# Performance work log

Hardware: AMD Instinct MI355X
Metric: run time of the kernel (lower is better)

Reference implementation:

```python
import jax, jax.numpy as jnp
import numpy as np

EPS = 1e-5  # torch InstanceNorm2d default eps


def setup_inputs() -> dict:
    key = jax.random.key(0)
    ks = jax.random.split(key, 5)
    B, C, H, W = 4, 64, 64, 64
    x = jax.random.normal(ks[0], (B, C, H, W), dtype=jnp.float32)
    # Conv2d 1x1 weights as [out_c, in_c] matrices (kernel dims squeezed)
    w_qkv = jax.random.normal(ks[1], (3 * C, C), dtype=jnp.float32) * (C ** -0.5)
    b_qkv = jax.random.normal(ks[2], (3 * C,), dtype=jnp.float32) * 0.02
    w_proj = jax.random.normal(ks[3], (C, C), dtype=jnp.float32) * (C ** -0.5)
    b_proj = jax.random.normal(ks[4], (C,), dtype=jnp.float32) * 0.02
    return {"x": x, "w_qkv": w_qkv, "b_qkv": b_qkv, "w_proj": w_proj, "b_proj": b_proj}


def reference(x, w_qkv, b_qkv, w_proj, b_proj):
    B, C, H, W = x.shape
    scale = C ** -0.5
    # InstanceNorm2d(affine=False): per-(B,C) stats over spatial dims, biased var
    mean = jnp.mean(x, axis=(2, 3), keepdims=True)
    var = jnp.var(x, axis=(2, 3), keepdims=True)
    h = (x - mean) * jax.lax.rsqrt(var + EPS)
    # 1x1 conv qkv projection: [B,3C,H,W]
    qkv = jnp.einsum('bchw,oc->bohw', h, w_qkv) + b_qkv[None, :, None, None]
    q, k, v = jnp.split(qkv, 3, axis=1)
    HW = H * W
    q = q.reshape(B, C, HW).transpose(0, 2, 1)  # [B, HW, C]
    k = k.reshape(B, C, HW)                      # [B, C, HW]
    v = v.reshape(B, C, HW).transpose(0, 2, 1)  # [B, HW, C]
    attn = jnp.einsum('bnc,bcm->bnm', q, k) * scale  # [B, HW, HW]
    attn = jax.nn.softmax(attn, axis=-1)
    # dropout p=0.0 -> identity
    h = jnp.einsum('bnm,bmc->bnc', attn, v)          # [B, HW, C]
    h = h.transpose(0, 2, 1).reshape(B, C, H, W)
    h = jnp.einsum('bchw,oc->bohw', h, w_proj) + b_proj[None, :, None, None]
    return x + h
```

## Files before the change

kernel.cpp:

```cpp
#include <hip/hip_runtime.h>
#include <hip/hip_bf16.h>

#define B_ 4
#define C_ 64
#define N_ 4096
#define EPS_ 1e-5f
#define C2_ 0.18033688011112042f

typedef __hip_bfloat16 bf16;
typedef __attribute__((ext_vector_type(8))) short short8;
typedef __attribute__((ext_vector_type(4))) short short4v;
typedef __attribute__((ext_vector_type(4))) float f32x4;

__device__ __forceinline__ float b2f(bf16 v) { return __bfloat162float(v); }

__device__ __forceinline__ short f2bs(float f) {
  union { bf16 h; short s; } u;
  u.h = __float2bfloat16(f);
  return u.s;
}

__device__ __forceinline__ short8 pk8(const float* f) {
  union { short8 v; short s[8]; } u;
#pragma unroll
  for (int i = 0; i < 8; ++i) u.s[i] = f2bs(f[i]);
  return u.v;
}

__device__ __forceinline__ void up8(short8 v, float* d) {
  union { short8 v; unsigned u[4]; } x;
  x.v = v;
  d[0] = __uint_as_float(x.u[0] << 16);
  d[1] = __uint_as_float(x.u[0] & 0xffff0000u);
  d[2] = __uint_as_float(x.u[1] << 16);
  d[3] = __uint_as_float(x.u[1] & 0xffff0000u);
  d[4] = __uint_as_float(x.u[2] << 16);
  d[5] = __uint_as_float(x.u[2] & 0xffff0000u);
  d[6] = __uint_as_float(x.u[3] << 16);
  d[7] = __uint_as_float(x.u[3] & 0xffff0000u);
}

__device__ __forceinline__ void up4(ushort4 u, float* d) {
  d[0] = __uint_as_float(((unsigned)u.x) << 16);
  d[1] = __uint_as_float(((unsigned)u.y) << 16);
  d[2] = __uint_as_float(((unsigned)u.z) << 16);
  d[3] = __uint_as_float(((unsigned)u.w) << 16);
}

template <bool F32>
__device__ __forceinline__ float ldx(const void* p, size_t idx) {
  if (F32) return ((const float*)p)[idx];
  return b2f(((const bf16*)p)[idx]);
}

template <bool F32>
__device__ __forceinline__ short8 ld8(const void* p, int idx) {
  if (F32) {
    const float* fp = (const float*)p + idx;
    float tmp[8];
    *(float4*)&tmp[0] = *(const float4*)fp;
    *(float4*)&tmp[4] = *(const float4*)(fp + 4);
    return pk8(tmp);
  }
  return *(const short8*)((const bf16*)p + idx);
}

__device__ __forceinline__ f32x4 mfma32(short8 a, short8 b, f32x4 c) {
  return __builtin_amdgcn_mfma_f32_16x16x32_bf16(a, b, c, 0, 0, 0);
}
__device__ __forceinline__ f32x4 mfma16(short4v a, short4v b, f32x4 c) {
  return __builtin_amdgcn_mfma_f32_16x16x16bf16_1k(a, b, c, 0, 0, 0);
}


template <bool F32>
__device__ __forceinline__ void stats_sum(const void* x, int bc, int t,
                                          float& s, float& s2) {
  if (F32) {
    const float4* xp = (const float4*)((const float*)x + (size_t)bc * N_);
#pragma unroll
    for (int r = 0; r < 4; ++r) {
      const float4 v = xp[r * 256 + t];
      s += (v.x + v.y) + (v.z + v.w);
      s2 += (v.x * v.x + v.y * v.y) + (v.z * v.z + v.w * v.w);
    }
  } else {
    const bf16* xp = (const bf16*)x + (size_t)bc * N_;
#pragma unroll
    for (int r = 0; r < 2; ++r) {
      float f[8];
      up8(*(const short8*)(xp + (r * 256 + t) * 8), f);
#pragma unroll
      for (int i = 0; i < 8; ++i) { s += f[i]; s2 += f[i] * f[i]; }
    }
  }
}

__global__ __launch_bounds__(256) void k_stats(const void* __restrict__ x,
                                               float* __restrict__ meanArr,
                                               float* __restrict__ rstdArr,
                                               int* __restrict__ flag) {
  const int bc = blockIdx.x, t = threadIdx.x;
  __shared__ float ps[4], ps2[4];
  __shared__ int pflag;
  {
    const ushort* xw = (const ushort*)x + (size_t)bc * 4096;
    int cnt = 0;
#pragma unroll
    for (int j = 0; j < 4; ++j) {
      const ushort4 u = *(const ushort4*)(xw + t * 16 + j * 4);
      cnt += ((u.x >> 7) & 0xFF) >= 143;
      cnt += ((u.y >> 7) & 0xFF) >= 143;
      cnt += ((u.z >> 7) & 0xFF) >= 143;
      cnt += ((u.w >> 7) & 0xFF) >= 143;
    }
#pragma unroll
    for (int off = 32; off > 0; off >>= 1) cnt += __shfl_down(cnt, off, 64);
    if (t == 0) pflag = 0;
    __syncthreads();
    if ((t & 63) == 0 && cnt > 16) atomicAdd(&pflag, cnt);
    __syncthreads();
  }
  const bool f32 = pflag > 64;
  float s = 0.f, s2 = 0.f;
  if (f32) stats_sum<true>(x, bc, t, s, s2);
  else stats_sum<false>(x, bc, t, s, s2);
#pragma unroll
  for (int off = 32; off > 0; off >>= 1) {
    s += __shfl_down(s, off, 64);
    s2 += __shfl_down(s2, off, 64);
  }
  if ((t & 63) == 0) { ps[t >> 6] = s; ps2[t >> 6] = s2; }
  __syncthreads();
  if (t == 0) {
    const float S = (ps[0] + ps[1]) + (ps[2] + ps[3]);
    const float S2 = (ps2[0] + ps2[1]) + (ps2[2] + ps2[3]);
    const float mean = S * (1.0f / N_);
    const float var = S2 * (1.0f / N_) - mean * mean;
    meanArr[bc] = mean;
    rstdArr[bc] = rsqrtf(var + EPS_);
    flag[0] = f32 ? 1 : 0;
  }
}

template <bool F32>
__device__ __forceinline__ void qkv_body(const void* x, const void* wqkv,
                                         const void* bqkv, const float* meanArr,
                                         const float* rstdArr, bf16* q, bf16* k,
                                         bf16* v, short* HB) {
  const int t = threadIdx.x, tj = blockIdx.x, b = blockIdx.y;
  const int n0 = tj * 64;
  {
    const int li = t & 15, nbt = (t >> 4) & 3, cg = t >> 6;
    const int n = n0 + nbt * 16 + li;
    const float* mb_ = meanArr + b * 64;
    const float* rb_ = rstdArr + b * 64;
    float hv[16];
#pragma unroll
    for (int i = 0; i < 16; ++i) {
      const int c = cg * 16 + i;
      hv[i] = (ldx<F32>(x, ((size_t)(b * 64 + c)) * N_ + n) - mb_[c]) * rb_[c];
    }
#pragma unroll
    for (int c8 = 0; c8 < 2; ++c8) {
      const int ks = cg >> 1, qd = (cg & 1) * 2 + c8;
      *(short8*)&HB[((nbt * 2 + ks) * 64 + qd * 16 + li) * 8] = pk8(&hv[c8 * 8]);
    }
  }
  __syncthreads();
  const int l = t & 63, w = t >> 6, li = l & 15, quad = l >> 4;
  short8 Wf[3][2];
#pragma unroll
  for (int sec = 0; sec < 3; ++sec)
#pragma unroll
    for (int ks = 0; ks < 2; ++ks)
      Wf[sec][ks] = ld8<F32>(wqkv, (sec * 64 + w * 16 + li) * 64 + ks * 32 + quad * 8);
  short8 Hf[4][2];
#pragma unroll
  for (int nb = 0; nb < 4; ++nb)
#pragma unroll
    for (int ks = 0; ks < 2; ++ks)
      Hf[nb][ks] = *(const short8*)&HB[((nb * 2 + ks) * 64 + l) * 8];
  float bq[4], bk[4];
#pragma unroll
  for (int r = 0; r < 4; ++r) {
    bq[r] = ldx<F32>(bqkv, w * 16 + quad * 4 + r);
    bk[r] = ldx<F32>(bqkv, 64 + w * 16 + quad * 4 + r);
  }
  const float bv = ldx<F32>(bqkv, 128 + w * 16 + li);
  const int lhi = ((w & 1) * 2 + (quad >> 1)) * 16 + li;
  const int jj0 = (quad & 1) * 4;
#pragma unroll
  for (int nb = 0; nb < 4; ++nb) {
    f32x4 dq = {0.f, 0.f, 0.f, 0.f}, dk = dq, dv = dq;
    dq = mfma32(Wf[0][0], Hf[nb][0], dq);
    dq = mfma32(Wf[0][1], Hf[nb][1], dq);
    dk = mfma32(Wf[1][0], Hf[nb][0], dk);
    dk = mfma32(Wf[1][1], Hf[nb][1], dk);
    dv = mfma32(Hf[nb][0], Wf[2][0], dv);
    dv = mfma32(Hf[nb][1], Wf[2][1], dv);
    union { ushort4 u; short s[4]; } pq, pk_, pv;
#pragma unroll
    for (int r = 0; r < 4; ++r) {
      pq.s[r] = f2bs(dq[r] + bq[r]);
      pk_.s[r] = f2bs(dk[r] + bk[r]);
      pv.s[r] = f2bs(dv[r] + bv);
    }
    *(ushort4*)&q[(((size_t)(b * 256 + tj * 4 + nb)) * 2 + (w >> 1)) * 512 + lhi * 8 + jj0] = pq.u;
    *(ushort4*)&k[(((size_t)(b * 64 + tj)) * 8 + nb * 2 + (w >> 1)) * 512 + lhi * 8 + jj0] = pk_.u;
    *(ushort4*)&v[(((size_t)(b * 64 + tj)) * 16 + w * 4 + nb) * 256 + (quad * 16 + li) * 4] = pv.u;
  }
}
__global__ __launch_bounds__(256) void k_qkv(
    const void* __restrict__ x, const void* __restrict__ wqkv,
    const void* __restrict__ bqkv, const float* __restrict__ meanArr,
    const float* __restrict__ rstdArr, bf16* __restrict__ q,
    bf16* __restrict__ k, bf16* __restrict__ v, const int* __restrict__ flag) {
  __shared__ short HB[4096];
  if (*flag) qkv_body<true>(x, wqkv, bqkv, meanArr, rstdArr, q, k, v, HB);
  else qkv_body<false>(x, wqkv, bqkv, meanArr, rstdArr, q, k, v, HB);
}

__device__ __forceinline__ void stage(short* dst, const bf16* ks_,
                                      const bf16* vs_, int w, int ln) {
#pragma unroll
  for (int i = 0; i < 2; ++i) {
    const int off = w * 1024 + i * 512;
    __builtin_amdgcn_global_load_lds(
        (const __attribute__((address_space(1))) unsigned int*)(ks_ + off + ln * 8),
        (__attribute__((address_space(3))) unsigned int*)(dst + off), 16, 0, 0);
    __builtin_amdgcn_global_load_lds(
        (const __attribute__((address_space(1))) unsigned int*)(vs_ + off + ln * 8),
        (__attribute__((address_space(3))) unsigned int*)(dst + 4096 + off), 16, 0, 0);
  }
}

__global__ __launch_bounds__(256, 2) void k_attn(
    const bf16* __restrict__ qg, const bf16* __restrict__ kg,
    const bf16* __restrict__ vg, bf16* __restrict__ opart,
    float* __restrict__ lpart) {
  __shared__ __align__(16) short KV[2][8192];
  const int bid = blockIdx.x;
  const int g = bid & 7, s = bid >> 3;
  const int c = g * 2 + (s & 1);
  const int b = c & 3, kh = c >> 2, qt = s >> 1;
  const int t = threadIdx.x, l = t & 63, w = t >> 6, li = l & 15, quad = l >> 4;

  short8 Qf[2][2];
#pragma unroll
  for (int q = 0; q < 2; ++q)
#pragma unroll
    for (int ks = 0; ks < 2; ++ks)
      Qf[q][ks] = *(const short8*)(qg +
          (((size_t)(b * 256 + qt * 8 + w * 2 + q)) * 2 + ks) * 512 + l * 8);

  f32x4 O[4][2];
#pragma unroll
  for (int cb = 0; cb < 4; ++cb)
#pragma unroll
    for (int q = 0; q < 2; ++q) O[cb][q] = {0.f, 0.f, 0.f, 0.f};
  float ls[2] = {0.f, 0.f};

  const bf16* kbase = kg + ((size_t)(b * 64 + kh * 16)) * 4096;
  const bf16* vbase = vg + ((size_t)(b * 64 + kh * 16)) * 4096;

  stage(&KV[0][0], kbase, vbase, w, l);
  __syncthreads();
  for (int it = 0; it < 16; ++it) {
    const short* buf = &KV[it & 1][0];
    if (it + 1 < 16)
      stage(&KV[(it + 1) & 1][0], kbase + (size_t)(it + 1) * 4096,
            vbase + (size_t)(it + 1) * 4096, w, l);
    short8 Kf[4][2];
#pragma unroll
    for (int jb = 0; jb < 4; ++jb)
#pragma unroll
      for (int ks = 0; ks < 2; ++ks)
        Kf[jb][ks] = *(const short8*)&buf[(jb * 2 + ks) * 512 + l * 8];
    short4v Vf[4][4];
#pragma unroll
    for (int cb = 0; cb < 4; ++cb)
#pragma unroll
      for (int jb = 0; jb < 4; ++jb)
        Vf[cb][jb] = *(const short4v*)&buf[4096 + (cb * 4 + jb) * 256 + l * 4];
#pragma unroll
    for (int jb = 0; jb < 4; ++jb) {
      short4v Pf[2];
#pragma unroll
      for (int q = 0; q < 2; ++q) {
        f32x4 sv = {0.f, 0.f, 0.f, 0.f};
        sv = mfma32(Kf[jb][0], Qf[q][0], sv);
        sv = mfma32(Kf[jb][1], Qf[q][1], sv);
        const float p0 = exp2f(sv[0] * C2_), p1 = exp2f(sv[1] * C2_);
        const float p2 = exp2f(sv[2] * C2_), p3 = exp2f(sv[3] * C2_);
        ls[q] += (p0 + p1) + (p2 + p3);
        union { short4v v; __hip_bfloat162 h[2]; } pu;
        pu.h[0] = __float22bfloat162_rn(make_float2(p0, p1));
        pu.h[1] = __float22bfloat162_rn(make_float2(p2, p3));
        Pf[q] = pu.v;
      }
#pragma unroll
      for (int cb = 0; cb < 4; ++cb)
#pragma unroll
        for (int q = 0; q < 2; ++q)
          O[cb][q] = mfma16(Vf[cb][jb], Pf[q], O[cb][q]);
    }
    __syncthreads();
  }
#pragma unroll
  for (int q = 0; q < 2; ++q) {
    ls[q] += __shfl_xor(ls[q], 16, 64);
    ls[q] += __shfl_xor(ls[q], 32, 64);
  }
  const size_t pb = ((size_t)(kh * 4 + b)) * 32 + qt;
  if (l < 16) {
    lpart[pb * 128 + (w * 2 + 0) * 16 + l] = ls[0];
    lpart[pb * 128 + (w * 2 + 1) * 16 + l] = ls[1];
  }
#pragma unroll
  for (int q = 0; q < 2; ++q)
#pragma unroll
    for (int cb = 0; cb < 4; ++cb) {
      union { ushort4 u; short s[4]; } pk_;
#pragma unroll
      for (int r = 0; r < 4; ++r) pk_.s[r] = f2bs(O[cb][q][r]);
      *(ushort4*)&opart[pb * 8192 + (((w * 2 + q) * 4 + cb) << 8) + l * 4] = pk_.u;
    }
}

template <bool F32>
__device__ __forceinline__ void proj_body(const bf16* opart, const float* lpart,
                                          const void* xg, const void* wp,
                                          const void* bp, void* outv) {
  const int qt64 = blockIdx.x, bb = blockIdx.y;
  const int qt = qt64 >> 1, mbo = (qt64 & 1) * 4;
  const int t = threadIdx.x, l = t & 63, w = t >> 6, li = l & 15, quad = l >> 4;
  short8 Wa[2];
#pragma unroll
  for (int ks = 0; ks < 2; ++ks)
    Wa[ks] = ld8<F32>(wp, (w * 16 + li) * 64 + ks * 32 + quad * 8);
  float bpv[4];
#pragma unroll
  for (int r = 0; r < 4; ++r) bpv[r] = ldx<F32>(bp, w * 16 + quad * 4 + r);
  f32x4 D[4];
#pragma unroll
  for (int mb = 0; mb < 4; ++mb) {
    const int mbg = mbo + mb;
    float lv = 0.f;
#pragma unroll
    for (int p = 0; p < 4; ++p)
      lv += lpart[(((size_t)(p * 4 + bb)) * 32 + qt) * 128 + mbg * 16 + li];
    lv = 1.0f / lv;
    f32x4 acc = {0.f, 0.f, 0.f, 0.f};
#pragma unroll
    for (int ks = 0; ks < 2; ++ks) {
      const int cb = ks * 2 + (quad >> 1);
      const int qs0 = (quad & 1) * 2;
      float s8[8] = {};
#pragma unroll
      for (int p = 0; p < 4; ++p) {
        const size_t base =
            (((size_t)(p * 4 + bb)) * 32 + qt) * 8192 + ((mbg * 4 + cb) << 8);
        float f0[4], f1[4];
        up4(*(const ushort4*)&opart[base + (qs0 * 16 + li) * 4], f0);
        up4(*(const ushort4*)&opart[base + ((qs0 + 1) * 16 + li) * 4], f1);
#pragma unroll
        for (int i = 0; i < 4; ++i) { s8[i] += f0[i]; s8[4 + i] += f1[i]; }
      }
#pragma unroll
      for (int i = 0; i < 8; ++i) s8[i] *= lv;
      acc = mfma32(Wa[ks], pk8(s8), acc);
    }
    D[mb] = acc;
  }
#pragma unroll
  for (int mb = 0; mb < 4; ++mb)
#pragma unroll
    for (int r = 0; r < 4; ++r) {
      const int o = w * 16 + quad * 4 + r;
      const int n = qt64 * 64 + mb * 16 + li;
      const size_t idx = ((size_t)(bb * 64 + o)) * N_ + n;
      const float res = ldx<F32>(xg, idx) + D[mb][r] + bpv[r];
      if (F32) ((float*)outv)[idx] = res;
      else ((bf16*)outv)[idx] = __float2bfloat16(res);
    }
}
__global__ __launch_bounds__(256) void k_proj(
    const bf16* __restrict__ opart, const float* __restrict__ lpart,
    const void* __restrict__ xg, const void* __restrict__ wp,
    const void* __restrict__ bp, void* __restrict__ outv,
    const int* __restrict__ flag) {
  if (*flag) proj_body<true>(opart, lpart, xg, wp, bp, outv);
  else proj_body<false>(opart, lpart, xg, wp, bp, outv);
}

extern "C" void kernel_launch(void* const* d_in, const int* in_sizes, int n_in,
                              void* d_out, int out_size, void* d_ws,
                              size_t ws_size, hipStream_t stream) {
  const void* x = d_in[0];
  const void* wqkv = d_in[1];
  const void* bqkv = d_in[2];
  const void* wproj = d_in[3];
  const void* bproj = d_in[4];

  char* ws = (char*)d_ws;
  float* meanArr = (float*)ws;
  float* rstdArr = (float*)(ws + 1024);
  int* flag = (int*)(ws + 2048);
  bf16* q = (bf16*)(ws + 4096);
  bf16* k = (bf16*)(ws + 4096 + (2u << 20));
  bf16* v = (bf16*)(ws + 4096 + (4u << 20));
  bf16* opart = (bf16*)(ws + 4096 + (6u << 20));
  float* lpart = (float*)(ws + 4096 + (14u << 20));

  k_stats<<<256, 256, 0, stream>>>(x, meanArr, rstdArr, flag);
  k_qkv<<<dim3(64, 4), 256, 0, stream>>>(x, wqkv, bqkv, meanArr, rstdArr, q, k,
                                         v, flag);
  k_attn<<<512, 256, 0, stream>>>(q, k, v, opart, lpart);
  k_proj<<<dim3(64, 4), 256, 0, stream>>>(opart, lpart, x, wproj, bproj, d_out,
                                          flag);
}
```

Measured before the change: 113.3 us.

## Double per-block query tile, split keys 8 ways, prescale Q, pack V loads

Each attention block now handles 64 queries per wave group (4 query fragments per wave) instead of 32, and the key dimension is split into 8 partitions of 512 keys instead of 4 of 1024. This doubles reuse of each K/V tile staged in LDS and halves the iterations per block. The softmax scale is folded into Q at projection time, which removes a multiply per score. V is stored so that 8-element LDS reads replace 4-element ones. The trade-off is more accumulator registers, which may cut occupancy, and twice as many partial outputs for the projection kernel to reduce.

```diff
diff --git a/kernel.cpp b/kernel.cpp
--- a/kernel.cpp
+++ b/kernel.cpp
@@ -202,13 +202,13 @@
     union { ushort4 u; short s[4]; } pq, pk_, pv;
 #pragma unroll
     for (int r = 0; r < 4; ++r) {
-      pq.s[r] = f2bs(dq[r] + bq[r]);
+      pq.s[r] = f2bs((dq[r] + bq[r]) * C2_);
       pk_.s[r] = f2bs(dk[r] + bk[r]);
       pv.s[r] = f2bs(dv[r] + bv);
     }
     *(ushort4*)&q[(((size_t)(b * 256 + tj * 4 + nb)) * 2 + (w >> 1)) * 512 + lhi * 8 + jj0] = pq.u;
     *(ushort4*)&k[(((size_t)(b * 64 + tj)) * 8 + nb * 2 + (w >> 1)) * 512 + lhi * 8 + jj0] = pk_.u;
-    *(ushort4*)&v[(((size_t)(b * 64 + tj)) * 16 + w * 4 + nb) * 256 + (quad * 16 + li) * 4] = pv.u;
+    *(ushort4*)&v[(((size_t)(b * 64 + tj)) * 8 + w * 2 + (nb >> 1)) * 512 + l * 8 + (nb & 1) * 4] = pv.u;
   }
 }
 __global__ __launch_bounds__(256) void k_qkv(
@@ -241,34 +241,33 @@
     float* __restrict__ lpart) {
   __shared__ __align__(16) short KV[2][8192];
   const int bid = blockIdx.x;
-  const int g = bid & 7, s = bid >> 3;
-  const int c = g * 2 + (s & 1);
-  const int b = c & 3, kh = c >> 2, qt = s >> 1;
+  const int kh = bid & 7, s = bid >> 3;
+  const int b = s & 3, qt = s >> 2;
   const int t = threadIdx.x, l = t & 63, w = t >> 6, li = l & 15, quad = l >> 4;
 
-  short8 Qf[2][2];
-#pragma unroll
-  for (int q = 0; q < 2; ++q)
+  short8 Qf[4][2];
+#pragma unroll
+  for (int q = 0; q < 4; ++q)
 #pragma unroll
     for (int ks = 0; ks < 2; ++ks)
       Qf[q][ks] = *(const short8*)(qg +
-          (((size_t)(b * 256 + qt * 8 + w * 2 + q)) * 2 + ks) * 512 + l * 8);
-
-  f32x4 O[4][2];
+          (((size_t)(b * 256 + qt * 16 + w * 4 + q)) * 2 + ks) * 512 + l * 8);
+
+  f32x4 O[4][4];
 #pragma unroll
   for (int cb = 0; cb < 4; ++cb)
 #pragma unroll
-    for (int q = 0; q < 2; ++q) O[cb][q] = {0.f, 0.f, 0.f, 0.f};
-  float ls[2] = {0.f, 0.f};
-
-  const bf16* kbase = kg + ((size_t)(b * 64 + kh * 16)) * 4096;
-  const bf16* vbase = vg + ((size_t)(b * 64 + kh * 16)) * 4096;
+    for (int q = 0; q < 4; ++q) O[cb][q] = {0.f, 0.f, 0.f, 0.f};
+  float ls[4] = {0.f, 0.f, 0.f, 0.f};
+
+  const bf16* kbase = kg + ((size_t)(b * 64 + kh * 8)) * 4096;
+  const bf16* vbase = vg + ((size_t)(b * 64 + kh * 8)) * 4096;
 
   stage(&KV[0][0], kbase, vbase, w, l);
   __syncthreads();
-  for (int it = 0; it < 16; ++it) {
+  for (int it = 0; it < 8; ++it) {
     const short* buf = &KV[it & 1][0];
-    if (it + 1 < 16)
+    if (it + 1 < 8)
       stage(&KV[(it + 1) & 1][0], kbase + (size_t)(it + 1) * 4096,
             vbase + (size_t)(it + 1) * 4096, w, l);
     short8 Kf[4][2];
@@ -277,22 +276,22 @@
 #pragma unroll
       for (int ks = 0; ks < 2; ++ks)
         Kf[jb][ks] = *(const short8*)&buf[(jb * 2 + ks) * 512 + l * 8];
-    short4v Vf[4][4];
+    short8 Vp[4][2];
 #pragma unroll
     for (int cb = 0; cb < 4; ++cb)
 #pragma unroll
-      for (int jb = 0; jb < 4; ++jb)
-        Vf[cb][jb] = *(const short4v*)&buf[4096 + (cb * 4 + jb) * 256 + l * 4];
+      for (int jp = 0; jp < 2; ++jp)
+        Vp[cb][jp] = *(const short8*)&buf[4096 + (cb * 2 + jp) * 512 + l * 8];
 #pragma unroll
     for (int jb = 0; jb < 4; ++jb) {
-      short4v Pf[2];
-#pragma unroll
-      for (int q = 0; q < 2; ++q) {
+      short4v Pf[4];
+#pragma unroll
+      for (int q = 0; q < 4; ++q) {
         f32x4 sv = {0.f, 0.f, 0.f, 0.f};
         sv = mfma32(Kf[jb][0], Qf[q][0], sv);
         sv = mfma32(Kf[jb][1], Qf[q][1], sv);
-        const float p0 = exp2f(sv[0] * C2_), p1 = exp2f(sv[1] * C2_);
-        const float p2 = exp2f(sv[2] * C2_), p3 = exp2f(sv[3] * C2_);
+        const float p0 = exp2f(sv[0]), p1 = exp2f(sv[1]);
+        const float p2 = exp2f(sv[2]), p3 = exp2f(sv[3]);
         ls[q] += (p0 + p1) + (p2 + p3);
         union { short4v v; __hip_bfloat162 h[2]; } pu;
         pu.h[0] = __float22bfloat162_rn(make_float2(p0, p1));
@@ -300,31 +299,36 @@
         Pf[q] = pu.v;
       }
 #pragma unroll
-      for (int cb = 0; cb < 4; ++cb)
-#pragma unroll
-        for (int q = 0; q < 2; ++q)
-          O[cb][q] = mfma16(Vf[cb][jb], Pf[q], O[cb][q]);
+      for (int cb = 0; cb < 4; ++cb) {
+        const short8 vp = Vp[cb][jb >> 1];
+        const short4v vh = (jb & 1)
+            ? __builtin_shufflevector(vp, vp, 4, 5, 6, 7)
+            : __builtin_shufflevector(vp, vp, 0, 1, 2, 3);
+#pragma unroll
+        for (int q = 0; q < 4; ++q) O[cb][q] = mfma16(vh, Pf[q], O[cb][q]);
+      }
     }
     __syncthreads();
   }
 #pragma unroll
-  for (int q = 0; q < 2; ++q) {
+  for (int q = 0; q < 4; ++q) {
     ls[q] += __shfl_xor(ls[q], 16, 64);
     ls[q] += __shfl_xor(ls[q], 32, 64);
   }
-  const size_t pb = ((size_t)(kh * 4 + b)) * 32 + qt;
+  const size_t pb = ((size_t)(kh * 4 + b)) * 16 + qt;
   if (l < 16) {
-    lpart[pb * 128 + (w * 2 + 0) * 16 + l] = ls[0];
-    lpart[pb * 128 + (w * 2 + 1) * 16 + l] = ls[1];
-  }
-#pragma unroll
-  for (int q = 0; q < 2; ++q)
+#pragma unroll
+    for (int q = 0; q < 4; ++q)
+      lpart[(pb * 16 + w * 4 + q) * 16 + l] = ls[q];
+  }
+#pragma unroll
+  for (int q = 0; q < 4; ++q)
 #pragma unroll
     for (int cb = 0; cb < 4; ++cb) {
       union { ushort4 u; short s[4]; } pk_;
 #pragma unroll
       for (int r = 0; r < 4; ++r) pk_.s[r] = f2bs(O[cb][q][r]);
-      *(ushort4*)&opart[pb * 8192 + (((w * 2 + q) * 4 + cb) << 8) + l * 4] = pk_.u;
+      *(ushort4*)&opart[((pb * 16 + w * 4 + q) * 4 + cb) * 256 + l * 4] = pk_.u;
     }
 }
 
@@ -333,7 +337,7 @@
                                           const void* xg, const void* wp,
                                           const void* bp, void* outv) {
   const int qt64 = blockIdx.x, bb = blockIdx.y;
-  const int qt = qt64 >> 1, mbo = (qt64 & 1) * 4;
+  const int qt = qt64 >> 2;
   const int t = threadIdx.x, l = t & 63, w = t >> 6, li = l & 15, quad = l >> 4;
   short8 Wa[2];
 #pragma unroll
@@ -345,11 +349,11 @@
   f32x4 D[4];
 #pragma unroll
   for (int mb = 0; mb < 4; ++mb) {
-    const int mbg = mbo + mb;
+    const int mbg = (qt64 & 3) * 4 + mb;
     float lv = 0.f;
 #pragma unroll
-    for (int p = 0; p < 4; ++p)
-      lv += lpart[(((size_t)(p * 4 + bb)) * 32 + qt) * 128 + mbg * 16 + li];
+    for (int p = 0; p < 8; ++p)
+      lv += lpart[((((size_t)(p * 4 + bb)) * 16 + qt) * 16 + mbg) * 16 + li];
     lv = 1.0f / lv;
     f32x4 acc = {0.f, 0.f, 0.f, 0.f};
 #pragma unroll
@@ -358,9 +362,9 @@
       const int qs0 = (quad & 1) * 2;
       float s8[8] = {};
 #pragma unroll
-      for (int p = 0; p < 4; ++p) {
+      for (int p = 0; p < 8; ++p) {
         const size_t base =
-            (((size_t)(p * 4 + bb)) * 32 + qt) * 8192 + ((mbg * 4 + cb) << 8);
+            (((((size_t)(p * 4 + bb)) * 16 + qt) * 16 + mbg) * 4 + cb) * 256;
         float f0[4], f1[4];
         up4(*(const ushort4*)&opart[base + (qs0 * 16 + li) * 4], f0);
         up4(*(const ushort4*)&opart[base + ((qs0 + 1) * 16 + li) * 4], f1);
@@ -411,7 +415,7 @@
   bf16* k = (bf16*)(ws + 4096 + (2u << 20));
   bf16* v = (bf16*)(ws + 4096 + (4u << 20));
   bf16* opart = (bf16*)(ws + 4096 + (6u << 20));
-  float* lpart = (float*)(ws + 4096 + (14u << 20));
+  float* lpart = (float*)(ws + 4096 + (23u << 20));
 
   k_stats<<<256, 256, 0, stream>>>(x, meanArr, rstdArr, flag);
   k_qkv<<<dim3(64, 4), 256, 0, stream>>>(x, wqkv, bqkv, meanArr, rstdArr, q, k,
```

Measured after the change: 119.5 us. +5.5%, slower.

## Split attention keys into eight chunks, fold softmax scale into Q, repack V

Applied to the files above, without the earlier changes.

The attention kernel now splits the key dimension into 8 partitions instead of 4, launching 1024 blocks with 8 iterations each and a higher occupancy hint. The softmax scale is folded into Q at projection time, which removes a multiply per score. V is stored in a packed 8-wide layout so each wave loads fewer, wider LDS vectors per pair of key blocks, and K fragments are loaded just in time to cut register pressure. The cost is larger partial-output buffers and twice as many partials for the projection kernel to reduce.

```diff
diff --git a/kernel.cpp b/kernel.cpp
--- a/kernel.cpp
+++ b/kernel.cpp
@@ -202,13 +202,13 @@
     union { ushort4 u; short s[4]; } pq, pk_, pv;
 #pragma unroll
     for (int r = 0; r < 4; ++r) {
-      pq.s[r] = f2bs(dq[r] + bq[r]);
+      pq.s[r] = f2bs((dq[r] + bq[r]) * C2_);
       pk_.s[r] = f2bs(dk[r] + bk[r]);
       pv.s[r] = f2bs(dv[r] + bv);
     }
     *(ushort4*)&q[(((size_t)(b * 256 + tj * 4 + nb)) * 2 + (w >> 1)) * 512 + lhi * 8 + jj0] = pq.u;
     *(ushort4*)&k[(((size_t)(b * 64 + tj)) * 8 + nb * 2 + (w >> 1)) * 512 + lhi * 8 + jj0] = pk_.u;
-    *(ushort4*)&v[(((size_t)(b * 64 + tj)) * 16 + w * 4 + nb) * 256 + (quad * 16 + li) * 4] = pv.u;
+    *(ushort4*)&v[(((size_t)(b * 64 + tj)) * 8 + w * 2 + (nb >> 1)) * 512 + l * 8 + (nb & 1) * 4] = pv.u;
   }
 }
 __global__ __launch_bounds__(256) void k_qkv(
@@ -235,16 +235,14 @@
   }
 }
 
-__global__ __launch_bounds__(256, 2) void k_attn(
+__global__ __launch_bounds__(256, 4) void k_attn(
     const bf16* __restrict__ qg, const bf16* __restrict__ kg,
     const bf16* __restrict__ vg, bf16* __restrict__ opart,
     float* __restrict__ lpart) {
   __shared__ __align__(16) short KV[2][8192];
   const int bid = blockIdx.x;
-  const int g = bid & 7, s = bid >> 3;
-  const int c = g * 2 + (s & 1);
-  const int b = c & 3, kh = c >> 2, qt = s >> 1;
-  const int t = threadIdx.x, l = t & 63, w = t >> 6, li = l & 15, quad = l >> 4;
+  const int kh = bid & 7, b = (bid >> 3) & 3, qt = bid >> 5;
+  const int t = threadIdx.x, l = t & 63, w = t >> 6, li = l & 15;
 
   short8 Qf[2][2];
 #pragma unroll
@@ -261,49 +259,50 @@
     for (int q = 0; q < 2; ++q) O[cb][q] = {0.f, 0.f, 0.f, 0.f};
   float ls[2] = {0.f, 0.f};
 
-  const bf16* kbase = kg + ((size_t)(b * 64 + kh * 16)) * 4096;
-  const bf16* vbase = vg + ((size_t)(b * 64 + kh * 16)) * 4096;
+  const bf16* kbase = kg + ((size_t)(b * 64 + kh * 8)) * 4096;
+  const bf16* vbase = vg + ((size_t)(b * 64 + kh * 8)) * 4096;
 
   stage(&KV[0][0], kbase, vbase, w, l);
   __syncthreads();
-  for (int it = 0; it < 16; ++it) {
+  for (int it = 0; it < 8; ++it) {
     const short* buf = &KV[it & 1][0];
-    if (it + 1 < 16)
+    if (it + 1 < 8)
       stage(&KV[(it + 1) & 1][0], kbase + (size_t)(it + 1) * 4096,
             vbase + (size_t)(it + 1) * 4096, w, l);
-    short8 Kf[4][2];
-#pragma unroll
-    for (int jb = 0; jb < 4; ++jb)
-#pragma unroll
-      for (int ks = 0; ks < 2; ++ks)
-        Kf[jb][ks] = *(const short8*)&buf[(jb * 2 + ks) * 512 + l * 8];
-    short4v Vf[4][4];
-#pragma unroll
-    for (int cb = 0; cb < 4; ++cb)
-#pragma unroll
-      for (int jb = 0; jb < 4; ++jb)
-        Vf[cb][jb] = *(const short4v*)&buf[4096 + (cb * 4 + jb) * 256 + l * 4];
-#pragma unroll
-    for (int jb = 0; jb < 4; ++jb) {
-      short4v Pf[2];
-#pragma unroll
-      for (int q = 0; q < 2; ++q) {
-        f32x4 sv = {0.f, 0.f, 0.f, 0.f};
-        sv = mfma32(Kf[jb][0], Qf[q][0], sv);
-        sv = mfma32(Kf[jb][1], Qf[q][1], sv);
-        const float p0 = exp2f(sv[0] * C2_), p1 = exp2f(sv[1] * C2_);
-        const float p2 = exp2f(sv[2] * C2_), p3 = exp2f(sv[3] * C2_);
-        ls[q] += (p0 + p1) + (p2 + p3);
-        union { short4v v; __hip_bfloat162 h[2]; } pu;
-        pu.h[0] = __float22bfloat162_rn(make_float2(p0, p1));
-        pu.h[1] = __float22bfloat162_rn(make_float2(p2, p3));
-        Pf[q] = pu.v;
+#pragma unroll
+    for (int jp = 0; jp < 2; ++jp) {
+      short8 Vp[4];
+#pragma unroll
+      for (int cb = 0; cb < 4; ++cb)
+        Vp[cb] = *(const short8*)&buf[4096 + (cb * 2 + jp) * 512 + l * 8];
+#pragma unroll
+      for (int jh = 0; jh < 2; ++jh) {
+        const int jb = jp * 2 + jh;
+        const short8 Kf0 = *(const short8*)&buf[(jb * 2 + 0) * 512 + l * 8];
+        const short8 Kf1 = *(const short8*)&buf[(jb * 2 + 1) * 512 + l * 8];
+        short4v Pf[2];
+#pragma unroll
+        for (int q = 0; q < 2; ++q) {
+          f32x4 sv = {0.f, 0.f, 0.f, 0.f};
+          sv = mfma32(Kf0, Qf[q][0], sv);
+          sv = mfma32(Kf1, Qf[q][1], sv);
+          const float p0 = exp2f(sv[0]), p1 = exp2f(sv[1]);
+          const float p2 = exp2f(sv[2]), p3 = exp2f(sv[3]);
+          ls[q] += (p0 + p1) + (p2 + p3);
+          union { short4v v; __hip_bfloat162 h[2]; } pu;
+          pu.h[0] = __float22bfloat162_rn(make_float2(p0, p1));
+          pu.h[1] = __float22bfloat162_rn(make_float2(p2, p3));
+          Pf[q] = pu.v;
+        }
+#pragma unroll
+        for (int cb = 0; cb < 4; ++cb) {
+          const short4v vh = jh
+              ? __builtin_shufflevector(Vp[cb], Vp[cb], 4, 5, 6, 7)
+              : __builtin_shufflevector(Vp[cb], Vp[cb], 0, 1, 2, 3);
+          O[cb][0] = mfma16(vh, Pf[0], O[cb][0]);
+          O[cb][1] = mfma16(vh, Pf[1], O[cb][1]);
+        }
       }
-#pragma unroll
-      for (int cb = 0; cb < 4; ++cb)
-#pragma unroll
-        for (int q = 0; q < 2; ++q)
-          O[cb][q] = mfma16(Vf[cb][jb], Pf[q], O[cb][q]);
     }
     __syncthreads();
   }
@@ -314,8 +313,9 @@
   }
   const size_t pb = ((size_t)(kh * 4 + b)) * 32 + qt;
   if (l < 16) {
-    lpart[pb * 128 + (w * 2 + 0) * 16 + l] = ls[0];
-    lpart[pb * 128 + (w * 2 + 1) * 16 + l] = ls[1];
+#pragma unroll
+    for (int q = 0; q < 2; ++q)
+      lpart[(pb * 8 + w * 2 + q) * 16 + l] = ls[q];
   }
 #pragma unroll
   for (int q = 0; q < 2; ++q)
@@ -324,7 +324,7 @@
       union { ushort4 u; short s[4]; } pk_;
 #pragma unroll
       for (int r = 0; r < 4; ++r) pk_.s[r] = f2bs(O[cb][q][r]);
-      *(ushort4*)&opart[pb * 8192 + (((w * 2 + q) * 4 + cb) << 8) + l * 4] = pk_.u;
+      *(ushort4*)&opart[((pb * 8 + w * 2 + q) * 4 + cb) * 256 + l * 4] = pk_.u;
     }
 }
 
@@ -333,7 +333,7 @@
                                           const void* xg, const void* wp,
                                           const void* bp, void* outv) {
   const int qt64 = blockIdx.x, bb = blockIdx.y;
-  const int qt = qt64 >> 1, mbo = (qt64 & 1) * 4;
+  const int qt = qt64 >> 1;
   const int t = threadIdx.x, l = t & 63, w = t >> 6, li = l & 15, quad = l >> 4;
   short8 Wa[2];
 #pragma unroll
@@ -345,11 +345,11 @@
   f32x4 D[4];
 #pragma unroll
   for (int mb = 0; mb < 4; ++mb) {
-    const int mbg = mbo + mb;
+    const int mbg = (qt64 & 1) * 4 + mb;
     float lv = 0.f;
 #pragma unroll
-    for (int p = 0; p < 4; ++p)
-      lv += lpart[(((size_t)(p * 4 + bb)) * 32 + qt) * 128 + mbg * 16 + li];
+    for (int p = 0; p < 8; ++p)
+      lv += lpart[((((size_t)(p * 4 + bb)) * 32 + qt) * 8 + mbg) * 16 + li];
     lv = 1.0f / lv;
     f32x4 acc = {0.f, 0.f, 0.f, 0.f};
 #pragma unroll
@@ -358,9 +358,9 @@
       const int qs0 = (quad & 1) * 2;
       float s8[8] = {};
 #pragma unroll
-      for (int p = 0; p < 4; ++p) {
+      for (int p = 0; p < 8; ++p) {
         const size_t base =
-            (((size_t)(p * 4 + bb)) * 32 + qt) * 8192 + ((mbg * 4 + cb) << 8);
+            (((((size_t)(p * 4 + bb)) * 32 + qt) * 8 + mbg) * 4 + cb) * 256;
         float f0[4], f1[4];
         up4(*(const ushort4*)&opart[base + (qs0 * 16 + li) * 4], f0);
         up4(*(const ushort4*)&opart[base + ((qs0 + 1) * 16 + li) * 4], f1);
@@ -411,12 +411,12 @@
   bf16* k = (bf16*)(ws + 4096 + (2u << 20));
   bf16* v = (bf16*)(ws + 4096 + (4u << 20));
   bf16* opart = (bf16*)(ws + 4096 + (6u << 20));
-  float* lpart = (float*)(ws + 4096 + (14u << 20));
+  float* lpart = (float*)(ws + 4096 + (22u << 20));
 
   k_stats<<<256, 256, 0, stream>>>(x, meanArr, rstdArr, flag);
   k_qkv<<<dim3(64, 4), 256, 0, stream>>>(x, wqkv, bqkv, meanArr, rstdArr, q, k,
                                          v, flag);
-  k_attn<<<512, 256, 0, stream>>>(q, k, v, opart, lpart);
+  k_attn<<<1024, 256, 0, stream>>>(q, k, v, opart, lpart);
   k_proj<<<dim3(64, 4), 256, 0, stream>>>(opart, lpart, x, wproj, bproj, d_out,
                                           flag);
 }
```

Result: no change. 113.5 us (+0.2%).
